# Performance work log

Measured on AMD Instinct MI355X. Metric: run time of the kernel, lower is better.

Reference implementation:

```python
import jax, jax.numpy as jnp
import numpy as np

N_NODES = 50000
N_EDGES = 800000
NODE_DIM = 128
EDGE_DIM = 64
OUT_DIM = 128
NEG_SLOPE = 0.2  # PyG GATConv default leaky_relu slope


def setup_inputs() -> dict:
    key = jax.random.key(0)
    ks = jax.random.split(key, 10)
    x = jax.random.normal(ks[0], (N_NODES, NODE_DIM), dtype=jnp.float32)
    edge_index = jax.random.randint(ks[1], (2, N_EDGES), 0, N_NODES, dtype=jnp.int64)
    edge_attr = jax.random.normal(ks[2], (N_EDGES, EDGE_DIM), dtype=jnp.float32)
    # edge_linear params
    We = jax.random.normal(ks[3], (EDGE_DIM, NODE_DIM), dtype=jnp.float32) / np.sqrt(EDGE_DIM)
    be = jnp.zeros((NODE_DIM,), dtype=jnp.float32)
    # GATConv(node_dim, out_dim, heads=1, concat=False) params
    Wg = jax.random.normal(ks[4], (NODE_DIM, OUT_DIM), dtype=jnp.float32) / np.sqrt(NODE_DIM)
    att_src = jax.random.normal(ks[5], (OUT_DIM,), dtype=jnp.float32) / np.sqrt(OUT_DIM)
    att_dst = jax.random.normal(ks[6], (OUT_DIM,), dtype=jnp.float32) / np.sqrt(OUT_DIM)
    bias = jnp.zeros((OUT_DIM,), dtype=jnp.float32)
    return {"x": x, "edge_index": edge_index, "edge_attr": edge_attr,
            "We": We, "be": be, "Wg": Wg, "att_src": att_src,
            "att_dst": att_dst, "bias": bias}


def reference(x, edge_index, edge_attr, We, be, Wg, att_src, att_dst, bias):
    N = x.shape[0]
    src, dst = edge_index[0], edge_index[1]

    # edge_linear + scatter_mean(edge_embedding, dst, dim_size=N)
    ee = edge_attr @ We + be  # [E, node_dim]
    sums = jax.ops.segment_sum(ee, dst, num_segments=N)
    cnt = jax.ops.segment_sum(jnp.ones((ee.shape[0],), ee.dtype), dst, num_segments=N)
    e2n = sums / jnp.maximum(cnt, 1.0)[:, None]
    x = x + e2n

    # GATConv(heads=1, concat=False, add_self_loops=True)
    h = x @ Wg  # [N, out_dim]
    loop = jnp.arange(N, dtype=src.dtype)
    s2 = jnp.concatenate([src, loop])  # edges + self-loops
    d2 = jnp.concatenate([dst, loop])
    a_s = h @ att_src  # [N]
    a_d = h @ att_dst  # [N]
    logits = jax.nn.leaky_relu(a_s[s2] + a_d[d2], NEG_SLOPE)  # [E+N]
    # segment softmax grouped by destination node
    seg_max = jax.ops.segment_max(logits, d2, num_segments=N)
    ex = jnp.exp(logits - seg_max[d2])
    den = jax.ops.segment_sum(ex, d2, num_segments=N)
    alpha = ex / den[d2]
    # weighted scatter-add of source messages
    out = jax.ops.segment_sum(alpha[:, None] * h[s2], d2, num_segments=N) + bias

    # graph readout
    return out.mean(axis=0)
```

## Files before the change

kernel.cpp:

```cpp
#include <hip/hip_runtime.h>

#define NODE_DIM 128
#define EDGE_DIM 64
#define OUT_DIM  128
#define NEG_SLOPE 0.2f
#define NREP 16
#define MAXDEG 64

__device__ __forceinline__ float leaky(float v) { return v > 0.f ? v : NEG_SLOPE * v; }

#define PRM_VS    0
#define PRM_VD    128
#define PRM_US    256
#define PRM_UD    320
#define PRM_CS    384
#define PRM_CD    385
#define PRM_S3    386
#define PRM_ACCXR 512
#define PRM_S64R  2560
#define PRM_SIZE  4096

__global__ __launch_bounds__(256) void k_zero(
    int* __restrict__ cnt, float* __restrict__ prm, int N)
{
    int i = blockIdx.x * 256 + threadIdx.x;
    if (i < N) cnt[i] = 0;
    if (i < PRM_SIZE) prm[i] = 0.f;
}

__global__ __launch_bounds__(256) void k_prep(
    const float* __restrict__ We, const float* __restrict__ be,
    const float* __restrict__ Wg, const float* __restrict__ att_src,
    const float* __restrict__ att_dst, float* __restrict__ prm)
{
    __shared__ float vs[128], vd[128];
    const int lane = threadIdx.x & 63, w = threadIdx.x >> 6;
    const float as0 = att_src[lane], as1 = att_src[64 + lane];
    const float ad0 = att_dst[lane], ad1 = att_dst[64 + lane];
    for (int r = w; r < NODE_DIM; r += 4) {
        const float w0 = Wg[r * OUT_DIM + lane], w1 = Wg[r * OUT_DIM + 64 + lane];
        float s = w0 * as0 + w1 * as1;
        float d = w0 * ad0 + w1 * ad1;
#pragma unroll
        for (int m = 32; m >= 1; m >>= 1) { s += __shfl_xor(s, m); d += __shfl_xor(d, m); }
        if (lane == 0) { vs[r] = s; vd[r] = d; prm[PRM_VS + r] = s; prm[PRM_VD + r] = d; }
    }
    __syncthreads();
    const float bv0 = vs[lane], bv1 = vs[64 + lane];
    const float bw0 = vd[lane], bw1 = vd[64 + lane];
    for (int r = w; r < EDGE_DIM; r += 4) {
        const float w0 = We[r * NODE_DIM + lane], w1 = We[r * NODE_DIM + 64 + lane];
        float us = w0 * bv0 + w1 * bv1;
        float ud = w0 * bw0 + w1 * bw1;
#pragma unroll
        for (int m = 32; m >= 1; m >>= 1) { us += __shfl_xor(us, m); ud += __shfl_xor(ud, m); }
        if (lane == 0) { prm[PRM_US + r] = us; prm[PRM_UD + r] = ud; }
    }
    if (w == 0) {
        const float b0 = be[lane], b1 = be[64 + lane];
        float cs = b0 * bv0 + b1 * bv1;
        float cd = b0 * bw0 + b1 * bw1;
#pragma unroll
        for (int m = 32; m >= 1; m >>= 1) { cs += __shfl_xor(cs, m); cd += __shfl_xor(cd, m); }
        if (lane == 0) { prm[PRM_CS] = cs; prm[PRM_CD] = cd; }
    }
}

__global__ __launch_bounds__(256) void k_csr(
    const int* __restrict__ idx, int* __restrict__ cnt, int* __restrict__ slots, int E)
{
    const int stride = gridDim.x * 256 * 4;
    for (int i0 = (blockIdx.x * 256 + threadIdx.x) * 4; i0 < E; i0 += stride) {
        if (i0 + 4 <= E) {
            const int4 d4 = *(const int4*)(idx + E + i0);
            int sl;
            sl = atomicAdd(&cnt[d4.x], 1); if (sl < MAXDEG) slots[(size_t)d4.x * MAXDEG + sl] = i0;
            sl = atomicAdd(&cnt[d4.y], 1); if (sl < MAXDEG) slots[(size_t)d4.y * MAXDEG + sl] = i0 + 1;
            sl = atomicAdd(&cnt[d4.z], 1); if (sl < MAXDEG) slots[(size_t)d4.z * MAXDEG + sl] = i0 + 2;
            sl = atomicAdd(&cnt[d4.w], 1); if (sl < MAXDEG) slots[(size_t)d4.w * MAXDEG + sl] = i0 + 3;
        } else {
            for (int i = i0; i < E; i++) {
                const int d = idx[E + i];
                const int sl = atomicAdd(&cnt[d], 1);
                if (sl < MAXDEG) slots[(size_t)d * MAXDEG + sl] = i;
            }
        }
    }
}

__global__ __launch_bounds__(256) void k_gatherA(
    const float* __restrict__ ea, const int* __restrict__ cnt, const int* __restrict__ slots,
    const float* __restrict__ x, const float* __restrict__ prm,
    float* __restrict__ rawsum, float* __restrict__ a_s, float* __restrict__ a_d, int N)
{
    const int lane = threadIdx.x & 63;
    const float us  = prm[PRM_US + lane];
    const float ud  = prm[PRM_UD + lane];
    const float vs0 = prm[PRM_VS + lane], vs1 = prm[PRM_VS + 64 + lane];
    const float vd0 = prm[PRM_VD + lane], vd1 = prm[PRM_VD + 64 + lane];
    const float cs = prm[PRM_CS], cd = prm[PRM_CD];
    const int wid = (blockIdx.x * 256 + threadIdx.x) >> 6;
    const int nw  = (gridDim.x * 256) >> 6;
    for (int n = wid; n < N; n += nw) {
        const int deg = min(cnt[n], MAXDEG);
        const int eid = slots[(size_t)n * MAXDEG + lane];
        const float x0 = x[(size_t)n * NODE_DIM + lane];
        const float x1 = x[(size_t)n * NODE_DIM + 64 + lane];
        float s0 = 0.f, s1 = 0.f, s2 = 0.f, s3 = 0.f;
        int i = 0;
        for (; i + 4 <= deg; i += 4) {
            const int e0 = __shfl(eid, i),     e1 = __shfl(eid, i + 1);
            const int e2 = __shfl(eid, i + 2), e3 = __shfl(eid, i + 3);
            s0 += ea[(size_t)e0 * EDGE_DIM + lane];
            s1 += ea[(size_t)e1 * EDGE_DIM + lane];
            s2 += ea[(size_t)e2 * EDGE_DIM + lane];
            s3 += ea[(size_t)e3 * EDGE_DIM + lane];
        }
        for (; i < deg; i++)
            s0 += ea[(size_t)__shfl(eid, i) * EDGE_DIM + lane];
        const float r = (s0 + s1) + (s2 + s3);
        rawsum[(size_t)n * EDGE_DIM + lane] = r;
        float ps = r * us, pd = r * ud;
        float gs = x0 * vs0 + x1 * vs1;
        float gd = x0 * vd0 + x1 * vd1;
#pragma unroll
        for (int m = 32; m >= 1; m >>= 1) {
            ps += __shfl_xor(ps, m); pd += __shfl_xor(pd, m);
            gs += __shfl_xor(gs, m); gd += __shfl_xor(gd, m);
        }
        if (lane == 0) {
            float as_ = gs, ad_ = gd;
            if (deg > 0) {
                const float ic = 1.f / (float)deg;
                as_ += ps * ic + cs;
                ad_ += pd * ic + cd;
            }
            a_s[n] = as_; a_d[n] = ad_;
        }
    }
}

__global__ __launch_bounds__(256) void k_denG(
    const int* __restrict__ idx, const int* __restrict__ cnt, const int* __restrict__ slots,
    const float* __restrict__ a_s, const float* __restrict__ a_d,
    float* __restrict__ rden, float* __restrict__ wsrc, int N)
{
    const int lane = threadIdx.x & 63;
    const int wid = (blockIdx.x * 256 + threadIdx.x) >> 6;
    const int nw  = (gridDim.x * 256) >> 6;
    for (int n = wid; n < N; n += 2 * nw) {
        const int n2 = n + nw;
        const int deg1 = min(cnt[n], MAXDEG);
        const float ad1 = a_d[n];
        float e1 = 0.f, e2 = 0.f;
        int deg2 = 0; float ad2 = 0.f;
        if (n2 < N) { deg2 = min(cnt[n2], MAXDEG); ad2 = a_d[n2]; }
        if (lane < deg1) {
            const int e = slots[(size_t)n * MAXDEG + lane];
            e1 = __expf(leaky(a_s[idx[e]] + ad1));
        }
        if (lane < deg2) {
            const int e = slots[(size_t)n2 * MAXDEG + lane];
            e2 = __expf(leaky(a_s[idx[e]] + ad2));
        }
#pragma unroll
        for (int m = 32; m >= 1; m >>= 1) { e1 += __shfl_xor(e1, m); e2 += __shfl_xor(e2, m); }
        if (lane == 0) {
            const float exS1 = __expf(leaky(a_s[n] + ad1));
            const float r1 = 1.f / (e1 + exS1);
            rden[n] = r1; wsrc[n] = exS1 * r1;
            if (n2 < N) {
                const float exS2 = __expf(leaky(a_s[n2] + ad2));
                const float r2 = 1.f / (e2 + exS2);
                rden[n2] = r2; wsrc[n2] = exS2 * r2;
            }
        }
    }
}

#define BIN_CH 8
#define BIN_SL 32
__global__ __launch_bounds__(1024) void k_binaccW(
    const int* __restrict__ idx, const float* __restrict__ a_s, const float* __restrict__ a_d,
    const float* __restrict__ rden, float* __restrict__ wsrc, int E, int N)
{
    __shared__ float lv[6272];
    const int chunk = (N + BIN_CH - 1) / BIN_CH;
    const int d0 = (int)(blockIdx.x & (BIN_CH - 1)) * chunk;
    const int nb = min(chunk, N - d0);
    for (int j = threadIdx.x; j < nb; j += 1024) lv[j] = 0.f;
    __syncthreads();
    const int es = blockIdx.x / BIN_CH;
    const int slice = (E + BIN_SL - 1) / BIN_SL;
    const int i1 = min(E, (es + 1) * slice);
    const int base = es * slice;
    for (int i0 = base + (int)threadIdx.x * 4; i0 < i1; i0 += 4096) {
        if (i0 + 4 <= i1) {
            const int4 s4 = *(const int4*)(idx + i0);
            const int4 d4 = *(const int4*)(idx + E + i0);
#pragma unroll
            for (int u = 0; u < 4; u++) {
                const int s = (&s4.x)[u], d = (&d4.x)[u];
                const unsigned r = (unsigned)(s - d0);
                if (r < (unsigned)nb) {
                    const float v = __expf(leaky(a_s[s] + a_d[d])) * rden[d];
                    atomicAdd(&lv[r], v);
                }
            }
        } else {
            for (int i = i0; i < i1; i++) {
                const int s = idx[i], d = idx[E + i];
                const unsigned r = (unsigned)(s - d0);
                if (r < (unsigned)nb) {
                    const float v = __expf(leaky(a_s[s] + a_d[d])) * rden[d];
                    atomicAdd(&lv[r], v);
                }
            }
        }
    }
    __syncthreads();
    for (int j = threadIdx.x; j < nb; j += 1024) {
        const float v = lv[j];
        if (v != 0.f) unsafeAtomicAdd(&wsrc[d0 + j], v);
    }
}

__global__ __launch_bounds__(256) void k_nodeB(
    const float* __restrict__ x, const float* __restrict__ rawsum,
    const float* __restrict__ wsrc, const int* __restrict__ cnt,
    float* __restrict__ prm, int N)
{
    __shared__ float sh[4][128];
    __shared__ float sh64[4][64];
    __shared__ float shs[4];
    const int lane = threadIdx.x & 63, w = threadIdx.x >> 6;
    const int wid = (blockIdx.x * 256 + threadIdx.x) >> 6;
    const int nw  = (gridDim.x * 256) >> 6;
    float a0 = 0.f, a1 = 0.f, r64 = 0.f, s3 = 0.f;
    for (int n = wid; n < N; n += 2 * nw) {
        const int n2 = n + nw;
        const float w1 = wsrc[n];
        const int   c1 = cnt[n];
        a0 += w1 * x[(size_t)n * NODE_DIM + lane];
        a1 += w1 * x[(size_t)n * NODE_DIM + 64 + lane];
        r64 += (w1 / (float)max(min(c1, MAXDEG), 1)) * rawsum[(size_t)n * EDGE_DIM + lane];
        if (lane == 0 && c1 > 0) s3 += w1;
        if (n2 < N) {
            const float w2 = wsrc[n2];
            const int   c2 = cnt[n2];
            a0 += w2 * x[(size_t)n2 * NODE_DIM + lane];
            a1 += w2 * x[(size_t)n2 * NODE_DIM + 64 + lane];
            r64 += (w2 / (float)max(min(c2, MAXDEG), 1)) * rawsum[(size_t)n2 * EDGE_DIM + lane];
            if (lane == 0 && c2 > 0) s3 += w2;
        }
    }
    sh[w][lane] = a0; sh[w][lane + 64] = a1;
    sh64[w][lane] = r64;
    if (lane == 0) shs[w] = s3;
    __syncthreads();
    const int t = threadIdx.x;
    if (t < 128) {
        float* dst = prm + PRM_ACCXR + (blockIdx.x & (NREP - 1)) * 128;
        unsafeAtomicAdd(&dst[t], sh[0][t] + sh[1][t] + sh[2][t] + sh[3][t]);
    }
    if (t < 64) {
        float* dst = prm + PRM_S64R + (blockIdx.x & (NREP - 1)) * 64;
        unsafeAtomicAdd(&dst[t], sh64[0][t] + sh64[1][t] + sh64[2][t] + sh64[3][t]);
    }
    if (t == 0)
        unsafeAtomicAdd(&prm[PRM_S3], shs[0] + shs[1] + shs[2] + shs[3]);
}

__global__ void k_final(const float* __restrict__ prm,
                        const float* __restrict__ We, const float* __restrict__ be,
                        const float* __restrict__ Wg, const float* __restrict__ bias,
                        float* __restrict__ out, float invN)
{
    __shared__ float s64[64], m[128];
    const int t = threadIdx.x;
    if (t < 64) {
        float s = 0.f;
        for (int r = 0; r < NREP; r++) s += prm[PRM_S64R + r * 64 + t];
        s64[t] = s;
    }
    float accx = 0.f;
    for (int r = 0; r < NREP; r++) accx += prm[PRM_ACCXR + r * 128 + t];
    __syncthreads();
    float t128 = 0.f;
    for (int j = 0; j < EDGE_DIM; j++) t128 += s64[j] * We[j * NODE_DIM + t];
    m[t] = accx + t128 + prm[PRM_S3] * be[t];
    __syncthreads();
    float o = 0.f;
    for (int k = 0; k < NODE_DIM; k++) o += m[k] * Wg[k * OUT_DIM + t];
    out[t] = o * invN + bias[t];
}

extern "C" void kernel_launch(void* const* d_in, const int* in_sizes, int n_in,
                              void* d_out, int out_size, void* d_ws, size_t ws_size,
                              hipStream_t stream)
{
    const float* x       = (const float*)d_in[0];
    const int*   idx     = (const int*)d_in[1];
    const float* ea      = (const float*)d_in[2];
    const float* We      = (const float*)d_in[3];
    const float* be      = (const float*)d_in[4];
    const float* Wg      = (const float*)d_in[5];
    const float* att_src = (const float*)d_in[6];
    const float* att_dst = (const float*)d_in[7];
    const float* bias    = (const float*)d_in[8];
    float* out = (float*)d_out;

    const int N = in_sizes[0] / NODE_DIM;
    const int E = in_sizes[1] / 2;

    float* prm    = (float*)d_ws;
    int*   cnt    = (int*)(prm + PRM_SIZE);
    float* a_s    = (float*)(cnt + N);
    float* a_d    = a_s + N;
    float* wsrc   = a_d + N;
    float* rden   = wsrc + N;
    int*   slots  = (int*)(rden + N);
    float* rawsum = (float*)(slots + (size_t)N * MAXDEG);

    k_zero   <<<(N + 255) / 256, 256, 0, stream>>>(cnt, prm, N);
    k_prep   <<<1, 256, 0, stream>>>(We, be, Wg, att_src, att_dst, prm);
    k_csr    <<<1024, 256, 0, stream>>>(idx, cnt, slots, E);
    k_gatherA<<<2048, 256, 0, stream>>>(ea, cnt, slots, x, prm, rawsum, a_s, a_d, N);
    k_denG   <<<1024, 256, 0, stream>>>(idx, cnt, slots, a_s, a_d, rden, wsrc, N);
    k_binaccW<<<BIN_CH * BIN_SL, 1024, 0, stream>>>(idx, a_s, a_d, rden, wsrc, E, N);
    k_nodeB  <<<512, 256, 0, stream>>>(x, rawsum, wsrc, cnt, prm, N);
    k_final  <<<1, 128, 0, stream>>>(prm, We, be, Wg, bias, out, 1.0f / N);
}
```

Measured before the change: 180.7 us.

## Store per-edge attention weights in denG and simplify binned scatter to key/value accumulation

The per-destination softmax kernel now writes each edge's normalized attention coefficient into a per-edge alpha array. The binned shared-memory accumulation then only streams source indices and alpha values instead of recomputing exp/leaky with random gathers of a_s, a_d and rden. This trades random gathers and exp work for an extra E-sized zeroing pass and a scattered write of alpha. Separately, the edge-attribute gather loop is unrolled to 8 accumulators to put more loads in flight.

```diff
diff --git a/kernel.cpp b/kernel.cpp
--- a/kernel.cpp
+++ b/kernel.cpp
@@ -21,11 +21,12 @@
 #define PRM_SIZE  4096
 
 __global__ __launch_bounds__(256) void k_zero(
-    int* __restrict__ cnt, float* __restrict__ prm, int N)
+    int* __restrict__ cnt, float* __restrict__ prm, float* __restrict__ alpha, int N, int E)
 {
     int i = blockIdx.x * 256 + threadIdx.x;
     if (i < N) cnt[i] = 0;
     if (i < PRM_SIZE) prm[i] = 0.f;
+    if (i < E) alpha[i] = 0.f;
 }
 
 __global__ __launch_bounds__(256) void k_prep(
@@ -107,7 +108,22 @@
         const float x0 = x[(size_t)n * NODE_DIM + lane];
         const float x1 = x[(size_t)n * NODE_DIM + 64 + lane];
         float s0 = 0.f, s1 = 0.f, s2 = 0.f, s3 = 0.f;
+        float s4 = 0.f, s5 = 0.f, s6 = 0.f, s7 = 0.f;
         int i = 0;
+        for (; i + 8 <= deg; i += 8) {
+            const int e0 = __shfl(eid, i),     e1 = __shfl(eid, i + 1);
+            const int e2 = __shfl(eid, i + 2), e3 = __shfl(eid, i + 3);
+            const int e4 = __shfl(eid, i + 4), e5 = __shfl(eid, i + 5);
+            const int e6 = __shfl(eid, i + 6), e7 = __shfl(eid, i + 7);
+            s0 += ea[(size_t)e0 * EDGE_DIM + lane];
+            s1 += ea[(size_t)e1 * EDGE_DIM + lane];
+            s2 += ea[(size_t)e2 * EDGE_DIM + lane];
+            s3 += ea[(size_t)e3 * EDGE_DIM + lane];
+            s4 += ea[(size_t)e4 * EDGE_DIM + lane];
+            s5 += ea[(size_t)e5 * EDGE_DIM + lane];
+            s6 += ea[(size_t)e6 * EDGE_DIM + lane];
+            s7 += ea[(size_t)e7 * EDGE_DIM + lane];
+        }
         for (; i + 4 <= deg; i += 4) {
             const int e0 = __shfl(eid, i),     e1 = __shfl(eid, i + 1);
             const int e2 = __shfl(eid, i + 2), e3 = __shfl(eid, i + 3);
@@ -118,7 +134,7 @@
         }
         for (; i < deg; i++)
             s0 += ea[(size_t)__shfl(eid, i) * EDGE_DIM + lane];
-        const float r = (s0 + s1) + (s2 + s3);
+        const float r = ((s0 + s1) + (s2 + s3)) + ((s4 + s5) + (s6 + s7));
         rawsum[(size_t)n * EDGE_DIM + lane] = r;
         float ps = r * us, pd = r * ud;
         float gs = x0 * vs0 + x1 * vs1;
@@ -143,7 +159,7 @@
 __global__ __launch_bounds__(256) void k_denG(
     const int* __restrict__ idx, const int* __restrict__ cnt, const int* __restrict__ slots,
     const float* __restrict__ a_s, const float* __restrict__ a_d,
-    float* __restrict__ rden, float* __restrict__ wsrc, int N)
+    float* __restrict__ alpha, float* __restrict__ wsrc, int N)
 {
     const int lane = threadIdx.x & 63;
     const int wid = (blockIdx.x * 256 + threadIdx.x) >> 6;
@@ -152,37 +168,39 @@
         const int n2 = n + nw;
         const int deg1 = min(cnt[n], MAXDEG);
         const float ad1 = a_d[n];
-        float e1 = 0.f, e2 = 0.f;
         int deg2 = 0; float ad2 = 0.f;
         if (n2 < N) { deg2 = min(cnt[n2], MAXDEG); ad2 = a_d[n2]; }
+        int es1 = 0, es2 = 0;
+        float x1v = 0.f, x2v = 0.f;
         if (lane < deg1) {
-            const int e = slots[(size_t)n * MAXDEG + lane];
-            e1 = __expf(leaky(a_s[idx[e]] + ad1));
+            es1 = slots[(size_t)n * MAXDEG + lane];
+            x1v = __expf(leaky(a_s[idx[es1]] + ad1));
         }
         if (lane < deg2) {
-            const int e = slots[(size_t)n2 * MAXDEG + lane];
-            e2 = __expf(leaky(a_s[idx[e]] + ad2));
-        }
+            es2 = slots[(size_t)n2 * MAXDEG + lane];
+            x2v = __expf(leaky(a_s[idx[es2]] + ad2));
+        }
+        float e1 = x1v, e2 = x2v;
 #pragma unroll
         for (int m = 32; m >= 1; m >>= 1) { e1 += __shfl_xor(e1, m); e2 += __shfl_xor(e2, m); }
-        if (lane == 0) {
-            const float exS1 = __expf(leaky(a_s[n] + ad1));
-            const float r1 = 1.f / (e1 + exS1);
-            rden[n] = r1; wsrc[n] = exS1 * r1;
-            if (n2 < N) {
-                const float exS2 = __expf(leaky(a_s[n2] + ad2));
-                const float r2 = 1.f / (e2 + exS2);
-                rden[n2] = r2; wsrc[n2] = exS2 * r2;
-            }
+        const float exS1 = __expf(leaky(a_s[n] + ad1));
+        const float r1 = 1.f / (e1 + exS1);
+        if (lane < deg1) alpha[es1] = x1v * r1;
+        if (lane == 0) wsrc[n] = exS1 * r1;
+        if (n2 < N) {
+            const float exS2 = __expf(leaky(a_s[n2] + ad2));
+            const float r2 = 1.f / (e2 + exS2);
+            if (lane < deg2) alpha[es2] = x2v * r2;
+            if (lane == 0) wsrc[n2] = exS2 * r2;
         }
     }
 }
 
 #define BIN_CH 8
 #define BIN_SL 32
-__global__ __launch_bounds__(1024) void k_binaccW(
-    const int* __restrict__ idx, const float* __restrict__ a_s, const float* __restrict__ a_d,
-    const float* __restrict__ rden, float* __restrict__ wsrc, int E, int N)
+__global__ __launch_bounds__(1024) void k_binacc(
+    const int* __restrict__ keys, const float* __restrict__ val,
+    float* __restrict__ outp, int E, int N)
 {
     __shared__ float lv[6272];
     const int chunk = (N + BIN_CH - 1) / BIN_CH;
@@ -196,32 +214,24 @@
     const int base = es * slice;
     for (int i0 = base + (int)threadIdx.x * 4; i0 < i1; i0 += 4096) {
         if (i0 + 4 <= i1) {
-            const int4 s4 = *(const int4*)(idx + i0);
-            const int4 d4 = *(const int4*)(idx + E + i0);
-#pragma unroll
-            for (int u = 0; u < 4; u++) {
-                const int s = (&s4.x)[u], d = (&d4.x)[u];
-                const unsigned r = (unsigned)(s - d0);
-                if (r < (unsigned)nb) {
-                    const float v = __expf(leaky(a_s[s] + a_d[d])) * rden[d];
-                    atomicAdd(&lv[r], v);
-                }
-            }
+            const int4   k4 = *(const int4*)(keys + i0);
+            const float4 v4 = *(const float4*)(val + i0);
+            unsigned r;
+            r = (unsigned)(k4.x - d0); if (r < (unsigned)nb) atomicAdd(&lv[r], v4.x);
+            r = (unsigned)(k4.y - d0); if (r < (unsigned)nb) atomicAdd(&lv[r], v4.y);
+            r = (unsigned)(k4.z - d0); if (r < (unsigned)nb) atomicAdd(&lv[r], v4.z);
+            r = (unsigned)(k4.w - d0); if (r < (unsigned)nb) atomicAdd(&lv[r], v4.w);
         } else {
             for (int i = i0; i < i1; i++) {
-                const int s = idx[i], d = idx[E + i];
-                const unsigned r = (unsigned)(s - d0);
-                if (r < (unsigned)nb) {
-                    const float v = __expf(leaky(a_s[s] + a_d[d])) * rden[d];
-                    atomicAdd(&lv[r], v);
-                }
+                const unsigned r = (unsigned)(keys[i] - d0);
+                if (r < (unsigned)nb) atomicAdd(&lv[r], val[i]);
             }
         }
     }
     __syncthreads();
     for (int j = threadIdx.x; j < nb; j += 1024) {
         const float v = lv[j];
-        if (v != 0.f) unsafeAtomicAdd(&wsrc[d0 + j], v);
+        if (v != 0.f) unsafeAtomicAdd(&outp[d0 + j], v);
     }
 }
 
@@ -318,16 +328,16 @@
     float* a_s    = (float*)(cnt + N);
     float* a_d    = a_s + N;
     float* wsrc   = a_d + N;
-    float* rden   = wsrc + N;
-    int*   slots  = (int*)(rden + N);
+    float* alpha  = wsrc + N;
+    int*   slots  = (int*)(alpha + E);
     float* rawsum = (float*)(slots + (size_t)N * MAXDEG);
 
-    k_zero   <<<(N + 255) / 256, 256, 0, stream>>>(cnt, prm, N);
+    k_zero   <<<(E + 255) / 256, 256, 0, stream>>>(cnt, prm, alpha, N, E);
     k_prep   <<<1, 256, 0, stream>>>(We, be, Wg, att_src, att_dst, prm);
     k_csr    <<<1024, 256, 0, stream>>>(idx, cnt, slots, E);
     k_gatherA<<<2048, 256, 0, stream>>>(ea, cnt, slots, x, prm, rawsum, a_s, a_d, N);
-    k_denG   <<<1024, 256, 0, stream>>>(idx, cnt, slots, a_s, a_d, rden, wsrc, N);
-    k_binaccW<<<BIN_CH * BIN_SL, 1024, 0, stream>>>(idx, a_s, a_d, rden, wsrc, E, N);
+    k_denG   <<<1024, 256, 0, stream>>>(idx, cnt, slots, a_s, a_d, alpha, wsrc, N);
+    k_binacc <<<BIN_CH * BIN_SL, 1024, 0, stream>>>(idx, alpha, wsrc, E, N);
     k_nodeB  <<<512, 256, 0, stream>>>(x, rawsum, wsrc, cnt, prm, N);
     k_final  <<<1, 128, 0, stream>>>(prm, We, be, Wg, bias, out, 1.0f / N);
 }
```

Result: no change. 183.8 us (+1.7%).
